# Optimization experiments

Hardware: AMD Instinct MI355X
Metric: run time of the kernel (lower is better)

The kernel has to match this reference:

```python
import jax, jax.numpy as jnp
import numpy as np
import math

IN_CH = 512
KEY_SIZE = 512
VALUE_SIZE = 512
B, T = 8, 2048


def setup_inputs() -> dict:
    key = jax.random.key(0)
    ks = jax.random.split(key, 7)
    s = 1.0 / math.sqrt(IN_CH)
    return {
        "x": jax.random.normal(ks[0], (B, T, IN_CH), dtype=jnp.float32),
        "Wq": jax.random.uniform(ks[1], (IN_CH, KEY_SIZE), jnp.float32, -s, s),
        "bq": jax.random.uniform(ks[2], (KEY_SIZE,), jnp.float32, -s, s),
        "Wk": jax.random.uniform(ks[3], (IN_CH, KEY_SIZE), jnp.float32, -s, s),
        "bk": jax.random.uniform(ks[4], (KEY_SIZE,), jnp.float32, -s, s),
        "Wv": jax.random.uniform(ks[5], (IN_CH, VALUE_SIZE), jnp.float32, -s, s),
        "bv": jax.random.uniform(ks[6], (VALUE_SIZE,), jnp.float32, -s, s),
    }


def reference(x, Wq, bq, Wk, bk, Wv, bv):
    # Projections (single head)
    q = jnp.einsum('btc,ck->btk', x, Wq) + bq  # [B,T,K]
    k = jnp.einsum('btc,ck->btk', x, Wk) + bk  # [B,T,K]
    v = jnp.einsum('btc,cv->btv', x, Wv) + bv  # [B,T,V]
    # Full score matrix, causal mask (strictly upper triangle masked: col > row)
    scores = jnp.einsum('bqk,btk->bqt', q, k)  # [B,T,T]
    t = scores.shape[1]
    causal = jnp.arange(t)[None, :] > jnp.arange(t)[:, None]  # True where future
    scores = jnp.where(causal[None], -jnp.inf, scores)
    attn = jax.nn.softmax(scores / math.sqrt(KEY_SIZE), axis=2)
    out = jnp.einsum('bqt,btv->bqv', attn, v)  # [B,T,V]
    return jnp.concatenate((x, out), axis=2)  # [B,T,C+V]
```

## Files before the change

### kernel.cpp

```cpp
#include <hip/hip_runtime.h>


#define DEV __device__ __forceinline__

typedef unsigned short u16;
typedef unsigned int u32;
typedef __attribute__((ext_vector_type(8))) short short8;
typedef __attribute__((ext_vector_type(4))) float float4v;

DEV u16 f2bf(float f) {
    u32 u = __float_as_uint(f);
    return (u16)((u + 0x7FFFu + ((u >> 16) & 1u)) >> 16);
}
DEV float bf2f(u16 h) { return __uint_as_float(((u32)h) << 16); }

DEV float4v mfma16(short8 a, short8 b, float4v c) {
    return __builtin_amdgcn_mfma_f32_16x16x32_bf16(a, b, c, 0, 0, 0);
}

#define GLD16(gptr, lptr)                                                     \
    __builtin_amdgcn_global_load_lds(                                         \
        (const __attribute__((address_space(1))) void*)(gptr),                \
        (__attribute__((address_space(3))) void*)(lptr), 16, 0, 0)

__global__ void detect_k(const u32* __restrict__ xw, int* __restrict__ flag) {
    __shared__ int sh[256];
    int tid = threadIdx.x;
    u32 w = xw[tid * 64];
    int e = (w >> 7) & 0xFF;
    sh[tid] = (e >= 0x60 && e <= 0x90) ? 1 : 0;
    __syncthreads();
    for (int s = 128; s > 0; s >>= 1) {
        if (tid < s) sh[tid] += sh[tid + s];
        __syncthreads();
    }
    if (tid == 0) flag[0] = (sh[0] > 128) ? 1 : 0;
}

__global__ void convx_k(const void* __restrict__ x, const int* __restrict__ flag,
                        u16* __restrict__ xb, void* __restrict__ out) {
    int i0 = (blockIdx.x * 256 + threadIdx.x) * 8;
    int row = i0 >> 9, col = i0 & 511;
    if (flag[0]) {
        uint4 v = *(const uint4*)((const u16*)x + i0);
        *(uint4*)&xb[i0] = v;
        *(uint4*)((u16*)out + (size_t)row * 1024 + col) = v;
    } else {
        const float* xf = (const float*)x;
        float4 f0 = *(const float4*)(xf + i0);
        float4 f1 = *(const float4*)(xf + i0 + 4);
        union { u16 us[8]; uint4 v; } pk;
        pk.us[0] = f2bf(f0.x); pk.us[1] = f2bf(f0.y);
        pk.us[2] = f2bf(f0.z); pk.us[3] = f2bf(f0.w);
        pk.us[4] = f2bf(f1.x); pk.us[5] = f2bf(f1.y);
        pk.us[6] = f2bf(f1.z); pk.us[7] = f2bf(f1.w);
        *(uint4*)&xb[i0] = pk.v;
        float* o = (float*)out + (size_t)row * 1024 + col;
        *(float4*)o = f0; *(float4*)(o + 4) = f1;
    }
}

__global__ void convwb_k(const void* __restrict__ Wq, const void* __restrict__ Wk,
                         const void* __restrict__ Wv, const void* __restrict__ bq,
                         const void* __restrict__ bk, const void* __restrict__ bv,
                         const int* __restrict__ flag,
                         u16* __restrict__ Wt, u16* __restrict__ bbuf) {
    int z = blockIdx.y;
    if (blockIdx.x >= 1024) {
        int i = (blockIdx.x - 1024) * 256 + threadIdx.x;
        const void* s = (z == 0) ? bq : ((z == 1) ? bk : bv);
        bbuf[z * 512 + i] = flag[0] ? ((const u16*)s)[i]
                                    : f2bf(((const float*)s)[i]);
        return;
    }
    const void* W = (z == 0) ? Wq : ((z == 1) ? Wk : Wv);
    int flat = blockIdx.x * 256 + threadIdx.x;
    int n = flat >> 9, k = flat & 511;
    u16 v = flag[0] ? ((const u16*)W)[k * 512 + n]
                    : f2bf(((const float*)W)[k * 512 + n]);
    Wt[z * 262144 + flat] = v;
}

#define PWB(N)                                                                \
    do {                                                                      \
        asm volatile("s_waitcnt vmcnt(" #N ")" ::: "memory");                 \
        __builtin_amdgcn_s_barrier();                                         \
        asm volatile("" ::: "memory");                                        \
    } while (0)

__global__ __launch_bounds__(256) void proj_k(
        const u16* __restrict__ x, const u16* __restrict__ Wt,
        const u16* __restrict__ bb,
        u16* __restrict__ Qo, u16* __restrict__ Ko, u16* __restrict__ Vt_out) {
    int z = blockIdx.z;
    const u16* Wz = Wt + z * 262144;
    const u16* bias = bb + z * 512;
    int mBase = blockIdx.x * 128;
    int nBase = blockIdx.y * 128;

    __shared__ __attribute__((aligned(16))) u16 Xs[2][128 * 32];
    __shared__ __attribute__((aligned(16))) u16 Ws[2][128 * 32];

    int tid = threadIdx.x;
    int w = tid >> 6, lane = tid & 63, quad = lane >> 4, l16 = lane & 15;
    int wr = (w >> 1) * 64, wc = (w & 1) * 64;

#define PISSUE(bi, k0)                                                        \
    { _Pragma("unroll")                                                       \
      for (int gg = 0; gg < 2; gg++) {                                        \
        int g = w * 2 + gg;                                                   \
        int row = g * 16 + (lane >> 2);                                       \
        int c8 = (lane & 3) ^ ((row >> 1) & 3);                               \
        GLD16(&x [(size_t)(mBase + row) * 512 + (k0) + c8 * 8], &Xs[bi][g * 512]); \
        GLD16(&Wz[(size_t)(nBase + row) * 512 + (k0) + c8 * 8], &Ws[bi][g * 512]); \
      } }

    PISSUE(0, 0)
    PISSUE(1, 32)

    float4v acc[4][4] = {};

    #pragma unroll 2
    for (int t = 0; t < 16; t++) {
        int bi = t & 1;
        if (t < 15) { PWB(4); } else { PWB(0); }

        short8 a[4], b[4];
        #pragma unroll
        for (int mt = 0; mt < 4; mt++) {
            int rr = wr + mt * 16 + l16;
            a[mt] = *(const short8*)&Xs[bi][rr * 32 + ((quad ^ ((rr >> 1) & 3)) * 8)];
        }
        #pragma unroll
        for (int nt = 0; nt < 4; nt++) {
            int rr = wc + nt * 16 + l16;
            b[nt] = *(const short8*)&Ws[bi][rr * 32 + ((quad ^ ((rr >> 1) & 3)) * 8)];
        }
        #pragma unroll
        for (int mt = 0; mt < 4; mt++)
            #pragma unroll
            for (int nt = 0; nt < 4; nt++)
                acc[mt][nt] = mfma16(a[mt], b[nt], acc[mt][nt]);

        if (t < 14) {
            asm volatile("s_waitcnt lgkmcnt(0)" ::: "memory");
            __builtin_amdgcn_s_barrier();
            asm volatile("" ::: "memory");
            PISSUE(bi, (t + 2) * 32)
        }
    }

    #pragma unroll
    for (int nt = 0; nt < 4; nt++) {
        int n = nBase + wc + nt * 16 + l16;
        float bval = bf2f(bias[n]);
        #pragma unroll
        for (int mt = 0; mt < 4; mt++) {
            int m0 = mBase + wr + mt * 16 + quad * 4;
            float4v v = acc[mt][nt];
            if (z == 2) {
                int bbi = m0 >> 11, tt = m0 & 2047;
                u16 t0 = f2bf(v[0] + bval), t1 = f2bf(v[1] + bval);
                u16 t2 = f2bf(v[2] + bval), t3 = f2bf(v[3] + bval);
                uint2 pk = make_uint2((u32)t0 | ((u32)t1 << 16), (u32)t2 | ((u32)t3 << 16));
                *(uint2*)&Vt_out[((size_t)bbi * 512 + n) * 2048 + tt] = pk;
            } else {
                u16* dst = (z == 0) ? Qo : Ko;
                #pragma unroll
                for (int r = 0; r < 4; r++)
                    dst[(size_t)(m0 + r) * 512 + n] = f2bf(v[r] + bval);
            }
        }
    }
}


#define LOADK(dst, kB, half)                                                  \
    { _Pragma("unroll")                                                       \
      for (int j = 0; j < 8; j++) {                                           \
        int row2 = 2 * (j * 4 + w);                                           \
        int row = row2 + (lane >> 5);                                         \
        int col8 = lane & 31;                                                 \
        GLD16(&Kb[(size_t)((kB) + row) * 512 + (half) * 256 +                 \
                  ((col8 ^ (row & 7)) << 3)], &dst[row2 * 256]);              \
      } }

#define LOADV(dst, kB, half)                                                  \
    { _Pragma("unroll")                                                       \
      for (int j = 0; j < 8; j++) {                                           \
        int blk8 = 8 * (j * 4 + w);                                           \
        int dl = blk8 + (lane >> 3);                                          \
        int col8 = lane & 7;                                                  \
        GLD16(&Vb[(size_t)((half) * 256 + dl) * 2048 + (kB) +                 \
                  ((col8 ^ (dl & 7)) << 3)], &dst[blk8 * 64]);                \
      } }

#define SSTEP(buf, h)                                                         \
    { _Pragma("unroll")                                                       \
      for (int kk = 0; kk < 8; kk++) {                                        \
        _Pragma("unroll")                                                     \
        for (int nt = 0; nt < 4; nt++) {                                      \
          short8 bf = *(const short8*)&buf[(nt * 16 + l16) * 256 +            \
                                           (((kk * 4 + quad) ^ sw) << 3)];    \
          accS[nt] = mfma16(qf[(h) * 8 + kk], bf, accS[nt]);                  \
        } } }

#define PVSTEP(buf, accO)                                                     \
    { _Pragma("unroll")                                                       \
      for (int kk = 0; kk < 2; kk++) {                                        \
        _Pragma("unroll")                                                     \
        for (int dt = 0; dt < 4; dt++) {                                      \
          int rowv = w * 64 + dt * 16 + l16;                                  \
          short8 bf = *(const short8*)&buf[rowv * 64 +                        \
                                           (((kk * 4 + quad) ^ sw) << 3)];    \
          _Pragma("unroll")                                                   \
          for (int mt = 0; mt < 4; mt++)                                      \
            accO[dt][mt] = mfma16(pf[mt][kk], bf, accO[dt][mt]);              \
        } } }

__global__ __launch_bounds__(256, 1) void attn_k(
        const u16* __restrict__ Q, const u16* __restrict__ K,
        const u16* __restrict__ Vt, const int* __restrict__ flag,
        void* __restrict__ out, u16* __restrict__ Opart,
        float2* __restrict__ ml, int dosplit) {
    int blk = blockIdx.x;
    int b, qt, h, kt0, kt1;
    if (dosplit) {
        qt = (blk < 256) ? (31 - (blk >> 4)) : ((blk - 256) >> 4);
        h  = (blk >> 3) & 1;
        b  = blk & 7;
        int n = qt + 1, mid = n >> 1;
        kt0 = h ? mid : 0;
        kt1 = h ? n : mid;
    } else {
        qt = 31 - (blk >> 3);
        h  = 0;
        b  = blk & 7;
        kt0 = 0; kt1 = qt + 1;
    }
    int q0 = qt * 64;
    int isbf = flag[0];

    __shared__ __attribute__((aligned(16))) u16 KV0[16384];
    __shared__ __attribute__((aligned(16))) u16 KV1[16384];
    __shared__ __attribute__((aligned(16))) u16 Ps[4096];
    __shared__ float al_s[64];
    __shared__ float il_s[64];
    __shared__ int skip_s[4];

    int tid = threadIdx.x;
    int w = tid >> 6, lane = tid & 63, quad = lane >> 4, l16 = lane & 15;
    int sw = l16 & 7;

    const u16* Qb = Q  + (size_t)b * 2048 * 512;
    const u16* Kb = K  + (size_t)b * 2048 * 512;
    const u16* Vb = Vt + (size_t)b * 512 * 2048;

    if (kt0 < kt1) LOADK(KV0, kt0 * 64, 0);

    short8 qf[16];
    {
        const u16* Qrow = &Qb[(size_t)(q0 + w * 16 + l16) * 512];
        #pragma unroll
        for (int g = 0; g < 16; g++)
            qf[g] = *(const short8*)&Qrow[g * 32 + quad * 8];
    }

    float4v accO0[4][4] = {};
    float4v accO1[4][4] = {};
    float4v accS[4] = {};
    short8 pf[4][2];
    float mrow[4] = {-1e30f, -1e30f, -1e30f, -1e30f};
    float lrow[4] = {0.f, 0.f, 0.f, 0.f};
    const float scale = 0.044194173824159216f;

    __syncthreads();

    for (int kt = kt0; kt < kt1; kt++) {
        int kB = kt * 64;

        LOADK(KV1, kB, 1);
        SSTEP(KV0, 0);
        __syncthreads();

        LOADV(KV0, kB, 0);
        SSTEP(KV1, 1);
        {
            int diag = (kt == qt);
            float pv[4][4], mx4[4], alpha[4];
            #pragma unroll
            for (int r = 0; r < 4; r++) {
                float mx = -1e30f;
                #pragma unroll
                for (int nt = 0; nt < 4; nt++) {
                    float sv = accS[nt][r] * scale;
                    if (diag && (nt * 16 + l16 > w * 16 + quad * 4 + r)) sv = -1e30f;
                    pv[nt][r] = sv;
                    mx = fmaxf(mx, sv);
                }
                mx = fmaxf(mx, __shfl_xor(mx, 1));
                mx = fmaxf(mx, __shfl_xor(mx, 2));
                mx = fmaxf(mx, __shfl_xor(mx, 4));
                mx = fmaxf(mx, __shfl_xor(mx, 8));
                mx4[r] = mx;
            }
            int small = (mx4[0] - mrow[0] <= 8.f) && (mx4[1] - mrow[1] <= 8.f) &&
                        (mx4[2] - mrow[2] <= 8.f) && (mx4[3] - mrow[3] <= 8.f);
            int wskip = __all(small) ? 1 : 0;
            if (lane == 0) skip_s[w] = wskip;
            #pragma unroll
            for (int r = 0; r < 4; r++) {
                float mnew = wskip ? mrow[r] : fmaxf(mrow[r], mx4[r]);
                float a = wskip ? 1.0f : __expf(mrow[r] - mnew);
                float sum = 0.f;
                #pragma unroll
                for (int nt = 0; nt < 4; nt++) {
                    pv[nt][r] = __expf(pv[nt][r] - mnew);
                    sum += pv[nt][r];
                }
                sum += __shfl_xor(sum, 1);
                sum += __shfl_xor(sum, 2);
                sum += __shfl_xor(sum, 4);
                sum += __shfl_xor(sum, 8);
                lrow[r] = lrow[r] * a + sum;
                mrow[r] = mnew;
                alpha[r] = a;
            }
            #pragma unroll
            for (int nt = 0; nt < 4; nt++)
                #pragma unroll
                for (int r = 0; r < 4; r++)
                    Ps[(w * 16 + quad * 4 + r) * 64 + nt * 16 + l16] = f2bf(pv[nt][r]);
            #pragma unroll
            for (int r = 0; r < 4; r++) al_s[w * 16 + quad * 4 + r] = alpha[r];
            #pragma unroll
            for (int nt = 0; nt < 4; nt++) accS[nt] = (float4v){0.f, 0.f, 0.f, 0.f};
        }
        __syncthreads();

        LOADV(KV1, kB, 1);
        {
            #pragma unroll
            for (int mt = 0; mt < 4; mt++)
                #pragma unroll
                for (int kk = 0; kk < 2; kk++)
                    pf[mt][kk] = *(const short8*)&Ps[(mt * 16 + l16) * 64 +
                                                     kk * 32 + quad * 8];
            int bskip = skip_s[0] & skip_s[1] & skip_s[2] & skip_s[3];
            if (!bskip) {
                float alf[4][4];
                #pragma unroll
                for (int mt = 0; mt < 4; mt++)
                    #pragma unroll
                    for (int r = 0; r < 4; r++)
                        alf[mt][r] = al_s[mt * 16 + quad * 4 + r];
                #pragma unroll
                for (int dt = 0; dt < 4; dt++)
                    #pragma unroll
                    for (int mt = 0; mt < 4; mt++)
                        #pragma unroll
                        for (int r = 0; r < 4; r++) {
                            accO0[dt][mt][r] *= alf[mt][r];
                            accO1[dt][mt][r] *= alf[mt][r];
                        }
            }
        }
        PVSTEP(KV0, accO0);
        __syncthreads();

        if (kt + 1 < kt1) LOADK(KV0, kB + 64, 0);
        PVSTEP(KV1, accO1);
        __syncthreads();
    }

    if (dosplit) {
        if (l16 == 0) {
            #pragma unroll
            for (int r = 0; r < 4; r++) {
                int grow = b * 2048 + q0 + w * 16 + quad * 4 + r;
                ml[h * 16384 + grow] = make_float2(mrow[r], lrow[r]);
            }
        }
        #pragma unroll
        for (int dt = 0; dt < 4; dt++) {
            int dg = w * 64 + dt * 16 + l16;
            #pragma unroll
            for (int mt = 0; mt < 4; mt++)
                #pragma unroll
                for (int r = 0; r < 4; r++) {
                    int grow = b * 2048 + q0 + mt * 16 + quad * 4 + r;
                    size_t base = ((size_t)h * 16384 + grow) * 512;
                    Opart[base + dg]       = f2bf(accO0[dt][mt][r]);
                    Opart[base + dg + 256] = f2bf(accO1[dt][mt][r]);
                }
        }
    } else {
        #pragma unroll
        for (int r = 0; r < 4; r++) il_s[w * 16 + quad * 4 + r] = 1.0f / lrow[r];
        __syncthreads();
        float invl[4][4];
        #pragma unroll
        for (int mt = 0; mt < 4; mt++)
            #pragma unroll
            for (int r = 0; r < 4; r++) invl[mt][r] = il_s[mt * 16 + quad * 4 + r];
        u16*   o16 = (u16*)out;
        float* o32 = (float*)out;
        #pragma unroll
        for (int dt = 0; dt < 4; dt++) {
            int dg0 = 512 + w * 64 + dt * 16 + l16;
            #pragma unroll
            for (int mt = 0; mt < 4; mt++)
                #pragma unroll
                for (int r = 0; r < 4; r++) {
                    int rowg = q0 + mt * 16 + quad * 4 + r;
                    size_t base = ((size_t)b * 2048 + rowg) * 1024;
                    float v0 = accO0[dt][mt][r] * invl[mt][r];
                    float v1 = accO1[dt][mt][r] * invl[mt][r];
                    if (isbf) {
                        o16[base + dg0]       = f2bf(v0);
                        o16[base + dg0 + 256] = f2bf(v1);
                    } else {
                        o32[base + dg0]       = v0;
                        o32[base + dg0 + 256] = v1;
                    }
                }
        }
    }
}

__global__ __launch_bounds__(256) void combine_k(
        const u16* __restrict__ Opart, const float2* __restrict__ ml,
        const int* __restrict__ flag, void* __restrict__ out) {
    int tid = threadIdx.x;
    int grow = blockIdx.x * 4 + (tid >> 6);
    int d0 = (tid & 63) * 8;
    float2 ml0 = ml[grow], ml1 = ml[16384 + grow];
    float m = fmaxf(ml0.x, ml1.x);
    float a0 = __expf(ml0.x - m), a1 = __expf(ml1.x - m);
    float il = 1.0f / (ml0.y * a0 + ml1.y * a1);
    a0 *= il; a1 *= il;
    uint4 v0 = *(const uint4*)&Opart[(size_t)grow * 512 + d0];
    uint4 v1 = *(const uint4*)&Opart[(size_t)(16384 + grow) * 512 + d0];
    const u16* u0 = (const u16*)&v0;
    const u16* u1 = (const u16*)&v1;
    float res[8];
    #pragma unroll
    for (int i = 0; i < 8; i++)
        res[i] = bf2f(u0[i]) * a0 + bf2f(u1[i]) * a1;
    size_t base = (size_t)grow * 1024 + 512 + d0;
    if (flag[0]) {
        union { u16 us[8]; uint4 v; } pk;
        #pragma unroll
        for (int i = 0; i < 8; i++) pk.us[i] = f2bf(res[i]);
        *(uint4*)((u16*)out + base) = pk.v;
    } else {
        float* o = (float*)out + base;
        *(float4*)o = make_float4(res[0], res[1], res[2], res[3]);
        *(float4*)(o + 4) = make_float4(res[4], res[5], res[6], res[7]);
    }
}

extern "C" void kernel_launch(void* const* d_in, const int* in_sizes, int n_in,
                              void* d_out, int out_size, void* d_ws, size_t ws_size,
                              hipStream_t stream) {
    const void* x  = d_in[0];
    const void* Wq = d_in[1];
    const void* bq = d_in[2];
    const void* Wk = d_in[3];
    const void* bk = d_in[4];
    const void* Wv = d_in[5];
    const void* bv = d_in[6];

    u16* base = (u16*)d_ws;
    int* flag = (int*)base;
    u16* Wt   = base + 8;
    u16* bb   = Wt + 786432;
    u16* xb   = bb + 1544;
    u16* Qw   = xb + 8388608;
    u16* Kw   = Qw + 8388608;
    u16* Vtw  = Kw + 8388608;
    u16* Opart = Vtw + 8388608;
    float2* mlb = (float2*)(Opart + 16777216);

    size_t need = ((size_t)(Opart - base) + 16777216) * 2 + 262144;
    int dosplit = (ws_size >= need) ? 1 : 0;

    hipLaunchKernelGGL(detect_k, dim3(1), dim3(256), 0, stream, (const u32*)x, flag);
    hipLaunchKernelGGL(convx_k, dim3(4096), dim3(256), 0, stream, x, flag, xb, d_out);
    hipLaunchKernelGGL(convwb_k, dim3(1026, 3), dim3(256), 0, stream,
                       Wq, Wk, Wv, bq, bk, bv, flag, Wt, bb);
    hipLaunchKernelGGL(proj_k, dim3(128, 4, 3), dim3(256), 0, stream, xb, Wt, bb, Qw, Kw, Vtw);
    if (dosplit) {
        hipLaunchKernelGGL(attn_k, dim3(512), dim3(256), 0, stream,
                           Qw, Kw, Vtw, flag, d_out, Opart, mlb, 1);
        hipLaunchKernelGGL(combine_k, dim3(4096), dim3(256), 0, stream,
                           Opart, mlb, flag, d_out);
    } else {
        hipLaunchKernelGGL(attn_k, dim3(256), dim3(256), 0, stream,
                           Qw, Kw, Vtw, flag, d_out, Opart, mlb, 0);
    }
}
```

Measured before the change: 286.0 us.

## Merge prep kernels, compute softmax row sums via MFMA, use hardware bf16 convert

Folds the dtype-detection, x-conversion and weight/bias transpose kernels into one prep kernel. Each block now detects the input dtype itself with a wave ballot, which removes two launches and the serial reduction. In the attention loop, the per-row softmax denominator is accumulated with extra MFMAs against a ones vector instead of the shuffle reductions. Software bf16 rounding is replaced with the v_cvt_pk_bf16_f32 instruction. The sum is now taken over the bf16-rounded probabilities, and each block re-detects the dtype from a smaller sample.

```diff
diff --git a/kernel.cpp b/kernel.cpp
--- a/kernel.cpp
+++ b/kernel.cpp
@@ -14,6 +14,12 @@
 }
 DEV float bf2f(u16 h) { return __uint_as_float(((u32)h) << 16); }
 
+DEV u16 f2bf1(float f) {
+    u32 r;
+    asm("v_cvt_pk_bf16_f32 %0, %1, %2" : "=v"(r) : "v"(f), "v"(f));
+    return (u16)r;
+}
+
 DEV float4v mfma16(short8 a, short8 b, float4v c) {
     return __builtin_amdgcn_mfma_f32_16x16x32_bf16(a, b, c, 0, 0, 0);
 }
@@ -23,61 +29,60 @@
         (const __attribute__((address_space(1))) void*)(gptr),                \
         (__attribute__((address_space(3))) void*)(lptr), 16, 0, 0)
 
-__global__ void detect_k(const u32* __restrict__ xw, int* __restrict__ flag) {
-    __shared__ int sh[256];
-    int tid = threadIdx.x;
-    u32 w = xw[tid * 64];
-    int e = (w >> 7) & 0xFF;
-    sh[tid] = (e >= 0x60 && e <= 0x90) ? 1 : 0;
-    __syncthreads();
-    for (int s = 128; s > 0; s >>= 1) {
-        if (tid < s) sh[tid] += sh[tid + s];
-        __syncthreads();
-    }
-    if (tid == 0) flag[0] = (sh[0] > 128) ? 1 : 0;
-}
-
-__global__ void convx_k(const void* __restrict__ x, const int* __restrict__ flag,
-                        u16* __restrict__ xb, void* __restrict__ out) {
-    int i0 = (blockIdx.x * 256 + threadIdx.x) * 8;
-    int row = i0 >> 9, col = i0 & 511;
-    if (flag[0]) {
-        uint4 v = *(const uint4*)((const u16*)x + i0);
-        *(uint4*)&xb[i0] = v;
-        *(uint4*)((u16*)out + (size_t)row * 1024 + col) = v;
-    } else {
-        const float* xf = (const float*)x;
-        float4 f0 = *(const float4*)(xf + i0);
-        float4 f1 = *(const float4*)(xf + i0 + 4);
-        union { u16 us[8]; uint4 v; } pk;
-        pk.us[0] = f2bf(f0.x); pk.us[1] = f2bf(f0.y);
-        pk.us[2] = f2bf(f0.z); pk.us[3] = f2bf(f0.w);
-        pk.us[4] = f2bf(f1.x); pk.us[5] = f2bf(f1.y);
-        pk.us[6] = f2bf(f1.z); pk.us[7] = f2bf(f1.w);
-        *(uint4*)&xb[i0] = pk.v;
-        float* o = (float*)out + (size_t)row * 1024 + col;
-        *(float4*)o = f0; *(float4*)(o + 4) = f1;
-    }
-}
-
-__global__ void convwb_k(const void* __restrict__ Wq, const void* __restrict__ Wk,
-                         const void* __restrict__ Wv, const void* __restrict__ bq,
-                         const void* __restrict__ bk, const void* __restrict__ bv,
-                         const int* __restrict__ flag,
-                         u16* __restrict__ Wt, u16* __restrict__ bbuf) {
-    int z = blockIdx.y;
-    if (blockIdx.x >= 1024) {
-        int i = (blockIdx.x - 1024) * 256 + threadIdx.x;
+__global__ void prep_k(const void* __restrict__ x,
+                       const void* __restrict__ Wq, const void* __restrict__ Wk,
+                       const void* __restrict__ Wv, const void* __restrict__ bq,
+                       const void* __restrict__ bk, const void* __restrict__ bv,
+                       int* __restrict__ flag, u16* __restrict__ xb,
+                       void* __restrict__ out, u16* __restrict__ Wt,
+                       u16* __restrict__ bbuf) {
+    int lane = threadIdx.x & 63;
+    u32 ws = ((const u32*)x)[lane * 16];
+    int e = (ws >> 7) & 0xFF;
+    unsigned long long m = __ballot(e >= 0x60 && e <= 0x90);
+    int isbf = (__popcll(m) > 32) ? 1 : 0;
+
+    int bid = blockIdx.x;
+    if (bid == 0 && threadIdx.x == 0) flag[0] = isbf;
+
+    if (bid < 4096) {
+        int i0 = (bid * 256 + threadIdx.x) * 8;
+        int row = i0 >> 9, col = i0 & 511;
+        if (isbf) {
+            uint4 v = *(const uint4*)((const u16*)x + i0);
+            *(uint4*)&xb[i0] = v;
+            *(uint4*)((u16*)out + (size_t)row * 1024 + col) = v;
+        } else {
+            const float* xf = (const float*)x;
+            float4 f0 = *(const float4*)(xf + i0);
+            float4 f1 = *(const float4*)(xf + i0 + 4);
+            union { u16 us[8]; uint4 v; } pk;
+            pk.us[0] = f2bf(f0.x); pk.us[1] = f2bf(f0.y);
+            pk.us[2] = f2bf(f0.z); pk.us[3] = f2bf(f0.w);
+            pk.us[4] = f2bf(f1.x); pk.us[5] = f2bf(f1.y);
+            pk.us[6] = f2bf(f1.z); pk.us[7] = f2bf(f1.w);
+            *(uint4*)&xb[i0] = pk.v;
+            float* o = (float*)out + (size_t)row * 1024 + col;
+            *(float4*)o = f0; *(float4*)(o + 4) = f1;
+        }
+        return;
+    }
+
+    int rem = bid - 4096;
+    int z = rem / 1026;
+    int ix = rem - z * 1026;
+    if (ix >= 1024) {
+        int i = (ix - 1024) * 256 + threadIdx.x;
         const void* s = (z == 0) ? bq : ((z == 1) ? bk : bv);
-        bbuf[z * 512 + i] = flag[0] ? ((const u16*)s)[i]
-                                    : f2bf(((const float*)s)[i]);
+        bbuf[z * 512 + i] = isbf ? ((const u16*)s)[i]
+                                 : f2bf(((const float*)s)[i]);
         return;
     }
     const void* W = (z == 0) ? Wq : ((z == 1) ? Wk : Wv);
-    int flat = blockIdx.x * 256 + threadIdx.x;
+    int flat = ix * 256 + threadIdx.x;
     int n = flat >> 9, k = flat & 511;
-    u16 v = flag[0] ? ((const u16*)W)[k * 512 + n]
-                    : f2bf(((const float*)W)[k * 512 + n]);
+    u16 v = isbf ? ((const u16*)W)[k * 512 + n]
+                 : f2bf(((const float*)W)[k * 512 + n]);
     Wt[z * 262144 + flat] = v;
 }
 
@@ -266,12 +271,16 @@
             qf[g] = *(const short8*)&Qrow[g * 32 + quad * 8];
     }
 
+    short8 onesf;
+    #pragma unroll
+    for (int j = 0; j < 8; j++) onesf[j] = (short)0x3F80;
+
     float4v accO0[4][4] = {};
     float4v accO1[4][4] = {};
     float4v accS[4] = {};
+    float4v accL = {};
     short8 pf[4][2];
     float mrow[4] = {-1e30f, -1e30f, -1e30f, -1e30f};
-    float lrow[4] = {0.f, 0.f, 0.f, 0.f};
     const float scale = 0.044194173824159216f;
 
     __syncthreads();
@@ -311,26 +320,17 @@
             #pragma unroll
             for (int r = 0; r < 4; r++) {
                 float mnew = wskip ? mrow[r] : fmaxf(mrow[r], mx4[r]);
-                float a = wskip ? 1.0f : __expf(mrow[r] - mnew);
-                float sum = 0.f;
-                #pragma unroll
-                for (int nt = 0; nt < 4; nt++) {
+                alpha[r] = wskip ? 1.0f : __expf(mrow[r] - mnew);
+                #pragma unroll
+                for (int nt = 0; nt < 4; nt++)
                     pv[nt][r] = __expf(pv[nt][r] - mnew);
-                    sum += pv[nt][r];
-                }
-                sum += __shfl_xor(sum, 1);
-                sum += __shfl_xor(sum, 2);
-                sum += __shfl_xor(sum, 4);
-                sum += __shfl_xor(sum, 8);
-                lrow[r] = lrow[r] * a + sum;
                 mrow[r] = mnew;
-                alpha[r] = a;
             }
             #pragma unroll
             for (int nt = 0; nt < 4; nt++)
                 #pragma unroll
                 for (int r = 0; r < 4; r++)
-                    Ps[(w * 16 + quad * 4 + r) * 64 + nt * 16 + l16] = f2bf(pv[nt][r]);
+                    Ps[(w * 16 + quad * 4 + r) * 64 + nt * 16 + l16] = f2bf1(pv[nt][r]);
             #pragma unroll
             for (int r = 0; r < 4; r++) al_s[w * 16 + quad * 4 + r] = alpha[r];
             #pragma unroll
@@ -363,7 +363,11 @@
                             accO0[dt][mt][r] *= alf[mt][r];
                             accO1[dt][mt][r] *= alf[mt][r];
                         }
+                #pragma unroll
+                for (int r = 0; r < 4; r++) accL[r] *= alf[w][r];
             }
+            accL = mfma16(pf[w][0], onesf, accL);
+            accL = mfma16(pf[w][1], onesf, accL);
         }
         PVSTEP(KV0, accO0);
         __syncthreads();
@@ -378,7 +382,7 @@
             #pragma unroll
             for (int r = 0; r < 4; r++) {
                 int grow = b * 2048 + q0 + w * 16 + quad * 4 + r;
-                ml[h * 16384 + grow] = make_float2(mrow[r], lrow[r]);
+                ml[h * 16384 + grow] = make_float2(mrow[r], accL[r]);
             }
         }
         #pragma unroll
@@ -390,13 +394,13 @@
                 for (int r = 0; r < 4; r++) {
                     int grow = b * 2048 + q0 + mt * 16 + quad * 4 + r;
                     size_t base = ((size_t)h * 16384 + grow) * 512;
-                    Opart[base + dg]       = f2bf(accO0[dt][mt][r]);
-                    Opart[base + dg + 256] = f2bf(accO1[dt][mt][r]);
+                    Opart[base + dg]       = f2bf1(accO0[dt][mt][r]);
+                    Opart[base + dg + 256] = f2bf1(accO1[dt][mt][r]);
                 }
         }
     } else {
         #pragma unroll
-        for (int r = 0; r < 4; r++) il_s[w * 16 + quad * 4 + r] = 1.0f / lrow[r];
+        for (int r = 0; r < 4; r++) il_s[w * 16 + quad * 4 + r] = 1.0f / accL[r];
         __syncthreads();
         float invl[4][4];
         #pragma unroll
@@ -417,8 +421,8 @@
                     float v0 = accO0[dt][mt][r] * invl[mt][r];
                     float v1 = accO1[dt][mt][r] * invl[mt][r];
                     if (isbf) {
-                        o16[base + dg0]       = f2bf(v0);
-                        o16[base + dg0 + 256] = f2bf(v1);
+                        o16[base + dg0]       = f2bf1(v0);
+                        o16[base + dg0 + 256] = f2bf1(v1);
                     } else {
                         o32[base + dg0]       = v0;
                         o32[base + dg0 + 256] = v1;
@@ -485,10 +489,8 @@
     size_t need = ((size_t)(Opart - base) + 16777216) * 2 + 262144;
     int dosplit = (ws_size >= need) ? 1 : 0;
 
-    hipLaunchKernelGGL(detect_k, dim3(1), dim3(256), 0, stream, (const u32*)x, flag);
-    hipLaunchKernelGGL(convx_k, dim3(4096), dim3(256), 0, stream, x, flag, xb, d_out);
-    hipLaunchKernelGGL(convwb_k, dim3(1026, 3), dim3(256), 0, stream,
-                       Wq, Wk, Wv, bq, bk, bv, flag, Wt, bb);
+    hipLaunchKernelGGL(prep_k, dim3(7174), dim3(256), 0, stream,
+                       x, Wq, Wk, Wv, bq, bk, bv, flag, xb, d_out, Wt, bb);
     hipLaunchKernelGGL(proj_k, dim3(128, 4, 3), dim3(256), 0, stream, xb, Wt, bb, Qw, Kw, Vtw);
     if (dosplit) {
         hipLaunchKernelGGL(attn_k, dim3(512), dim3(256), 0, stream,
```

Result: slower. 496.8 us (+73.7%).
